# Kernel optimization log

Hardware: AMD Instinct MI355X
Metric: run time of the kernel (lower is better)

## Reference

```python
import jax, jax.numpy as jnp
import numpy as np

D_P, D_T, D_F = 128, 256, 384
D = D_P + D_T + D_F            # 768
NUM_PART, NUM_TIMES, NUM_F0 = 64, 601, 360
NHEAD, NLAYERS, DFF = 12, 6, 2048
CTX, PRED = 1024, 64
BATCH = 8
NEG = -1e9


def sin_emb(vals, d, L, base=10000.0):
    # vectorized version of the per-scalar sin_embedding loop
    i = jnp.arange(d // 2, dtype=jnp.float32)
    wk = base ** (-i / d) * (d / L)
    ang = vals[..., None].astype(jnp.float32) * wk           # [..., d/2]
    return jnp.stack([jnp.sin(ang), jnp.cos(ang)], axis=-1).reshape(vals.shape + (d,))


def layernorm(x, g, b, eps=1e-5):
    mu = jnp.mean(x, axis=-1, keepdims=True)
    var = jnp.var(x, axis=-1, keepdims=True)
    return (x - mu) * jax.lax.rsqrt(var + eps) * g + b


def setup_inputs() -> dict:
    key = jax.random.key(0)
    ks = jax.random.split(key, 20)
    inp = {}
    inp['context_participant'] = jax.random.randint(ks[0], (BATCH, CTX), 0, NUM_PART)
    inp['context_time'] = jax.random.uniform(ks[1], (BATCH, CTX), jnp.float32) * 60.0
    inp['context_f0'] = jax.random.randint(ks[2], (BATCH, CTX), 0, NUM_F0)
    # learned / frozen tables
    inp['part_table'] = jax.random.normal(ks[3], (NUM_PART, D_P), jnp.float32)
    inp['time_table'] = sin_emb(jnp.arange(NUM_TIMES, dtype=jnp.float32), D_T, NUM_TIMES)
    inp['f0_table'] = sin_emb(jnp.arange(NUM_F0, dtype=jnp.float32), D_F, NUM_F0)
    inp['pad'] = jax.random.normal(ks[4], (D,), jnp.float32)
    s = 0.02
    inp['Wqkv'] = jax.random.normal(ks[5], (NLAYERS, 3 * D, D), jnp.float32) * s
    inp['bqkv'] = jnp.zeros((NLAYERS, 3 * D), jnp.float32)
    inp['Wo'] = jax.random.normal(ks[6], (NLAYERS, D, D), jnp.float32) * s
    inp['bo'] = jnp.zeros((NLAYERS, D), jnp.float32)
    inp['ln1_g'] = jnp.ones((NLAYERS, D), jnp.float32)
    inp['ln1_b'] = jnp.zeros((NLAYERS, D), jnp.float32)
    inp['W1'] = jax.random.normal(ks[7], (NLAYERS, DFF, D), jnp.float32) * s
    inp['b1'] = jnp.zeros((NLAYERS, DFF), jnp.float32)
    inp['W2'] = jax.random.normal(ks[8], (NLAYERS, D, DFF), jnp.float32) * s
    inp['b2'] = jnp.zeros((NLAYERS, D), jnp.float32)
    inp['ln2_g'] = jnp.ones((NLAYERS, D), jnp.float32)
    inp['ln2_b'] = jnp.zeros((NLAYERS, D), jnp.float32)
    return inp


def reference(context_participant, context_time, context_f0, part_table, time_table,
              f0_table, pad, Wqkv, bqkv, Wo, bo, ln1_g, ln1_b, W1, b1, W2, b2,
              ln2_g, ln2_b):
    B = context_participant.shape[0]
    emb = jnp.concatenate([
        part_table[context_participant],
        sin_emb(context_time, D_T, NUM_TIMES),
        f0_table[context_f0],
    ], axis=-1)                                               # [B, CTX, D]
    dummy = jnp.broadcast_to(pad[None, None, :], (B, PRED, D))
    x = jnp.concatenate([emb, dummy], axis=1)                 # [B, S, D]
    S = CTX + PRED
    # causal mask with -1e9 above diagonal; target block fully masked (incl. diag)
    mask = jnp.where(jnp.triu(jnp.ones((S, S), bool), k=1), NEG, 0.0).astype(jnp.float32)
    mask = mask.at[CTX:, CTX:].set(NEG)
    hd = D // NHEAD
    scale = 1.0 / jnp.sqrt(jnp.float32(hd))
    for l in range(NLAYERS):
        qkv = x @ Wqkv[l].T + bqkv[l]
        q, k, v = jnp.split(qkv, 3, axis=-1)
        q = q.reshape(B, S, NHEAD, hd)
        k = k.reshape(B, S, NHEAD, hd)
        v = v.reshape(B, S, NHEAD, hd)
        scores = jnp.einsum('bqhd,bkhd->bhqk', q, k) * scale + mask
        attn = jax.nn.softmax(scores, axis=-1)
        ctx = jnp.einsum('bhqk,bkhd->bqhd', attn, v).reshape(B, S, D)
        x = layernorm(x + (ctx @ Wo[l].T + bo[l]), ln1_g[l], ln1_b[l])
        ff = jax.nn.relu(x @ W1[l].T + b1[l]) @ W2[l].T + b2[l]
        x = layernorm(x + ff, ln2_g[l], ln2_b[l])
    pred = x[:, CTX:, :]
    pred_cat_logits = pred[:, :, :D_P] @ part_table.T
    pred_time_logits = pred[:, :, D_P:D_P + D_T] @ time_table.T
    pred_f0_logits = pred[:, :, D_P + D_T:] @ f0_table.T
    return (pred_cat_logits, pred_time_logits, pred_f0_logits)
```

## Files before the change

kernel.cpp:

```cpp
#include <hip/hip_runtime.h>
#include <hip/hip_bf16.h>
#include <math.h>

#define D_P 128
#define D_T 256
#define D_F 384
#define DIM 768
#define NUM_TIMES 601
#define NUM_F0 360
#define NHEAD 12
#define HD 64
#define NLAYERS 6
#define DFF 2048
#define CTX 1024
#define SEQ 1088
#define BATCH 8
#define ROWS (BATCH*SEQ)
#define TDIM3 (3*DIM)
#define PREDROWS 512

typedef unsigned short ushort_t;
typedef __attribute__((ext_vector_type(8))) short bfrag;
typedef __attribute__((ext_vector_type(4))) float f32x4;

__global__ void SequenceModel_30425548325019_kernel(unsigned short* out, int n, unsigned short v) {
  int i = blockIdx.x * 256 + threadIdx.x;
  if (i < n) out[i] = v;
}

__device__ inline short f2bf(float f) {
  unsigned u = __float_as_uint(f);
  unsigned r = (u + 0x7FFFu + ((u >> 16) & 1u)) >> 16;
  return (short)r;
}

__device__ inline void gload16(const void* g, void* l) {
  __builtin_amdgcn_global_load_lds(
      (const __attribute__((address_space(1))) unsigned*)g,
      (__attribute__((address_space(3))) unsigned*)l, 16, 0, 0);
}

__global__ __launch_bounds__(256) void cvt_bf16(const float* __restrict__ src,
                                                ushort_t* __restrict__ dst, int n) {
  int i = (blockIdx.x * 256 + threadIdx.x) * 4;
  if (i >= n) return;
  float4 v = *(const float4*)(src + i);
  dst[i + 0] = (ushort_t)f2bf(v.x);
  dst[i + 1] = (ushort_t)f2bf(v.y);
  dst[i + 2] = (ushort_t)f2bf(v.z);
  dst[i + 3] = (ushort_t)f2bf(v.w);
}

__global__ __launch_bounds__(256) void embed_kernel(
    const int* __restrict__ cp, const float* __restrict__ ct,
    const int* __restrict__ cf, const float* __restrict__ part,
    const float* __restrict__ f0t, const float* __restrict__ pad,
    float* __restrict__ x, ushort_t* __restrict__ xb) {
  int idx = blockIdx.x * 256 + threadIdx.x;
  if (idx >= ROWS * DIM) return;
  int d = idx % DIM;
  int row = idx / DIM;
  int b = row / SEQ, s = row - b * SEQ;
  float v;
  if (s >= CTX) {
    v = pad[d];
  } else if (d < D_P) {
    v = part[cp[b * CTX + s] * D_P + d];
  } else if (d < D_P + D_T) {
    int j = d - D_P;
    int i2 = j >> 1;
    float wk = powf(10000.f, -(float)i2 / (float)D_T) * ((float)D_T / (float)NUM_TIMES);
    float ang = ct[b * CTX + s] * wk;
    v = (j & 1) ? cosf(ang) : sinf(ang);
  } else {
    v = f0t[cf[b * CTX + s] * D_F + (d - D_P - D_T)];
  }
  x[idx] = v;
  xb[idx] = (ushort_t)f2bf(v);
}

#define BM 128
#define BN 128
#define BK 32

__global__ __launch_bounds__(256) void gemm_bb(
    const ushort_t* __restrict__ A, const ushort_t* __restrict__ B,
    const float* __restrict__ bias, const float* __restrict__ resid,
    float* __restrict__ C, ushort_t* __restrict__ Cb,
    int M, int N, int K, int relu, int qscale) {
  __shared__ short As[4 * BM * 8];
  __shared__ short Bs[4 * BN * 8];
  const int tid = threadIdx.x;
  const int wave = tid >> 6, lane = tid & 63;
  const int wr = wave >> 1, wc = wave & 1;
  const int l15 = lane & 15, l4 = lane >> 4;
  const int m0 = blockIdx.y * BM, n0 = blockIdx.x * BN;
  f32x4 acc[4][4] = {};

  for (int k0 = 0; k0 < K; k0 += BK) {
    __syncthreads();
    #pragma unroll
    for (int i = 0; i < 2; ++i) {
      int u = i * 256 + wave * 64 + lane;
      int row = u & 127, kg = u >> 7;
      gload16(A + (size_t)(m0 + row) * K + k0 + kg * 8, &As[(i * 256 + wave * 64) * 8]);
      gload16(B + (size_t)(n0 + row) * K + k0 + kg * 8, &Bs[(i * 256 + wave * 64) * 8]);
    }
    __syncthreads();
    bfrag a[4], b[4];
    #pragma unroll
    for (int f = 0; f < 4; ++f) {
      a[f] = *(const bfrag*)&As[(l4 * BM + wr * 64 + f * 16 + l15) * 8];
      b[f] = *(const bfrag*)&Bs[(l4 * BN + wc * 64 + f * 16 + l15) * 8];
    }
    #pragma unroll
    for (int i = 0; i < 4; ++i)
      #pragma unroll
      for (int j = 0; j < 4; ++j)
        acc[i][j] = __builtin_amdgcn_mfma_f32_16x16x32_bf16(a[i], b[j], acc[i][j], 0, 0, 0);
  }
  #pragma unroll
  for (int i = 0; i < 4; ++i) {
    int mbase = m0 + wr * 64 + i * 16 + l4 * 4;
    #pragma unroll
    for (int j = 0; j < 4; ++j) {
      int n = n0 + wc * 64 + j * 16 + l15;
      float bv = bias[n];
      #pragma unroll
      for (int r = 0; r < 4; ++r) {
        int m = mbase + r;
        float v = acc[i][j][r] + bv;
        if (resid) v += resid[(size_t)m * N + n];
        if (relu) v = fmaxf(v, 0.f);
        if (qscale && n < DIM) v *= 0.125f;
        if (C) C[(size_t)m * N + n] = v;
        if (Cb) Cb[(size_t)m * N + n] = (ushort_t)f2bf(v);
      }
    }
  }
}

__global__ __launch_bounds__(256) void gather_pred(const ushort_t* __restrict__ xb,
                                                   ushort_t* __restrict__ xpb) {
  int idx = blockIdx.x * 256 + threadIdx.x;
  if (idx >= PREDROWS * DIM) return;
  int r = idx / DIM, d = idx - r * DIM;
  int b = r >> 6, rr = r & 63;
  xpb[idx] = xb[(size_t)(b * SEQ + CTX + rr) * DIM + d];
}

__global__ __launch_bounds__(256) void head_mfma(
    const ushort_t* __restrict__ A, const ushort_t* __restrict__ B,
    float* __restrict__ C, int N, int K, int lda, int coloff) {
  __shared__ short As[4 * BM * 8];
  __shared__ short Bs[4 * BN * 8];
  const int tid = threadIdx.x;
  const int wave = tid >> 6, lane = tid & 63;
  const int wr = wave >> 1, wc = wave & 1;
  const int l15 = lane & 15, l4 = lane >> 4;
  const int m0 = blockIdx.y * BM, n0 = blockIdx.x * BN;
  f32x4 acc[4][4] = {};

  for (int k0 = 0; k0 < K; k0 += BK) {
    __syncthreads();
    #pragma unroll
    for (int i = 0; i < 2; ++i) {
      int u = i * 256 + wave * 64 + lane;
      int row = u & 127, kg = u >> 7;
      gload16(A + (size_t)(m0 + row) * lda + coloff + k0 + kg * 8,
              &As[(i * 256 + wave * 64) * 8]);
      gload16(B + (size_t)(n0 + row) * K + k0 + kg * 8,
              &Bs[(i * 256 + wave * 64) * 8]);
    }
    __syncthreads();
    bfrag a[4], b[4];
    #pragma unroll
    for (int f = 0; f < 4; ++f) {
      a[f] = *(const bfrag*)&As[(l4 * BM + wr * 64 + f * 16 + l15) * 8];
      b[f] = *(const bfrag*)&Bs[(l4 * BN + wc * 64 + f * 16 + l15) * 8];
    }
    #pragma unroll
    for (int i = 0; i < 4; ++i)
      #pragma unroll
      for (int j = 0; j < 4; ++j)
        acc[i][j] = __builtin_amdgcn_mfma_f32_16x16x32_bf16(a[i], b[j], acc[i][j], 0, 0, 0);
  }
  #pragma unroll
  for (int i = 0; i < 4; ++i) {
    int mbase = m0 + wr * 64 + i * 16 + l4 * 4;
    #pragma unroll
    for (int j = 0; j < 4; ++j) {
      int n = n0 + wc * 64 + j * 16 + l15;
      if (n >= N) continue;
      #pragma unroll
      for (int r = 0; r < 4; ++r)
        C[(size_t)(mbase + r) * N + n] = acc[i][j][r];
    }
  }
}

#define QBLK 64
#define KBLK 64
__global__ __launch_bounds__(256) void attn_mfma(const ushort_t* __restrict__ qkv,
                                                 ushort_t* __restrict__ outb) {
  const int qt = blockIdx.x, h = blockIdx.y, b = blockIdx.z;
  const int q0 = qt * QBLK;
  __shared__ short Vt[8 * 64 * 9];
  __shared__ short Ps[8 * 64 * 9];
  __shared__ float SO[64 * 65];
  __shared__ float alphaS[64], linvS[64];
  const int tid = threadIdx.x;
  const int wave = tid >> 6, lane = tid & 63;
  const int l15 = lane & 15, l4 = lane >> 4;
  const int smrow = tid >> 2, smc = tid & 3;
  const int qf = wave;

  const size_t qrow_addr = (size_t)(b * SEQ + q0 + qf * 16 + l15) * TDIM3 + h * HD;
  bfrag aq0 = *(const bfrag*)(qkv + qrow_addr + 0 * 32 + l4 * 8);
  bfrag aq1 = *(const bfrag*)(qkv + qrow_addr + 1 * 32 + l4 * 8);

  float mrun = -1e30f, lrun = 0.f;
  f32x4 o[4] = {};
  const int nkt = (q0 < CTX) ? (q0 + QBLK) / KBLK : (CTX / KBLK);

  for (int kt = 0; kt < nkt; ++kt) {
    const int k0 = kt * KBLK;
    __syncthreads();
    #pragma unroll
    for (int i = 0; i < 2; ++i) {
      int u = tid + 256 * i;
      int krow = u >> 3, dg = u & 7;
      bfrag vv = *(const bfrag*)(qkv + (size_t)(b * SEQ + k0 + krow) * TDIM3 + 2 * DIM + h * HD + dg * 8);
      int kg = krow >> 3, j = krow & 7;
      #pragma unroll
      for (int e = 0; e < 8; ++e)
        Vt[(kg * 64 + dg * 8 + e) * 9 + j] = vv[e];
    }
    #pragma unroll
    for (int jk = 0; jk < 4; ++jk) {
      const size_t krow_addr = (size_t)(b * SEQ + k0 + jk * 16 + l15) * TDIM3 + DIM + h * HD;
      bfrag bk0 = *(const bfrag*)(qkv + krow_addr + 0 * 32 + l4 * 8);
      bfrag bk1 = *(const bfrag*)(qkv + krow_addr + 1 * 32 + l4 * 8);
      f32x4 s = {};
      s = __builtin_amdgcn_mfma_f32_16x16x32_bf16(aq0, bk0, s, 0, 0, 0);
      s = __builtin_amdgcn_mfma_f32_16x16x32_bf16(aq1, bk1, s, 0, 0, 0);
      #pragma unroll
      for (int r = 0; r < 4; ++r)
        SO[(qf * 16 + l4 * 4 + r) * 65 + jk * 16 + l15] = s[r];
    }
    __syncthreads();
    {
      const int qglob = q0 + smrow;
      float p[16];
      float tm = -1e30f;
      #pragma unroll
      for (int i = 0; i < 16; ++i) {
        int kg = k0 + smc * 16 + i;
        float s = SO[smrow * 65 + smc * 16 + i];
        bool allowed = (qglob < CTX) ? (kg <= qglob) : true;
        p[i] = allowed ? s : -1e30f;
        tm = fmaxf(tm, p[i]);
      }
      tm = fmaxf(tm, __shfl_xor(tm, 1));
      tm = fmaxf(tm, __shfl_xor(tm, 2));
      float mn = fmaxf(mrun, tm);
      float alpha = __expf(mrun - mn);
      float ls = 0.f;
      #pragma unroll
      for (int i = 0; i < 16; ++i) { p[i] = __expf(p[i] - mn); ls += p[i]; }
      ls += __shfl_xor(ls, 1);
      ls += __shfl_xor(ls, 2);
      lrun = lrun * alpha + ls;
      mrun = mn;
      if (smc == 0) alphaS[smrow] = alpha;
      short* pd0 = &Ps[((smc * 2 + 0) * 64 + smrow) * 9];
      short* pd1 = &Ps[((smc * 2 + 1) * 64 + smrow) * 9];
      #pragma unroll
      for (int i = 0; i < 8; ++i) { pd0[i] = f2bf(p[i]); pd1[i] = f2bf(p[i + 8]); }
    }
    __syncthreads();
    {
      #pragma unroll
      for (int r = 0; r < 4; ++r) {
        float ar = alphaS[qf * 16 + l4 * 4 + r];
        #pragma unroll
        for (int df = 0; df < 4; ++df) o[df][r] *= ar;
      }
      #pragma unroll
      for (int c = 0; c < 2; ++c) {
        bfrag pa = *(const bfrag*)&Ps[((c * 4 + l4) * 64 + qf * 16 + l15) * 9];
        #pragma unroll
        for (int df = 0; df < 4; ++df) {
          bfrag v = *(const bfrag*)&Vt[((c * 4 + l4) * 64 + df * 16 + l15) * 9];
          o[df] = __builtin_amdgcn_mfma_f32_16x16x32_bf16(pa, v, o[df], 0, 0, 0);
        }
      }
    }
  }
  if (smc == 0) linvS[smrow] = 1.f / lrun;
  __syncthreads();
  #pragma unroll
  for (int r = 0; r < 4; ++r) {
    float li = linvS[qf * 16 + l4 * 4 + r];
    #pragma unroll
    for (int df = 0; df < 4; ++df)
      SO[(qf * 16 + l4 * 4 + r) * 65 + df * 16 + l15] = o[df][r] * li;
  }
  __syncthreads();
  #pragma unroll
  for (int i = 0; i < 2; ++i) {
    int s = tid + 256 * i;
    int r = s >> 3, kg = s & 7;
    ushort_t* dst = outb + (size_t)(b * SEQ + q0 + r) * DIM + h * HD + kg * 8;
    const float* sp = &SO[r * 65 + kg * 8];
    bfrag t;
    #pragma unroll
    for (int e = 0; e < 8; ++e) t[e] = f2bf(sp[e]);
    *(bfrag*)dst = t;
  }
}

__global__ __launch_bounds__(256) void ln_kernel(float* __restrict__ x,
                                                 const float* __restrict__ g,
                                                 const float* __restrict__ bb,
                                                 ushort_t* __restrict__ xb) {
  const int row = blockIdx.x;
  float* p = x + (size_t)row * DIM;
  ushort_t* pb = xb + (size_t)row * DIM;
  const int tid = threadIdx.x;
  float v0 = p[tid], v1 = p[tid + 256], v2 = p[tid + 512];
  float s1 = v0 + v1 + v2;
  float s2 = v0 * v0 + v1 * v1 + v2 * v2;
  #pragma unroll
  for (int off = 32; off >= 1; off >>= 1) {
    s1 += __shfl_down(s1, off);
    s2 += __shfl_down(s2, off);
  }
  __shared__ float r1[4], r2[4];
  int wid = tid >> 6;
  if ((tid & 63) == 0) { r1[wid] = s1; r2[wid] = s2; }
  __syncthreads();
  s1 = r1[0] + r1[1] + r1[2] + r1[3];
  s2 = r2[0] + r2[1] + r2[2] + r2[3];
  const float mu = s1 * (1.f / DIM);
  const float var = s2 * (1.f / DIM) - mu * mu;
  const float rs = rsqrtf(var + 1e-5f);
  float o0 = (v0 - mu) * rs * g[tid]       + bb[tid];
  float o1 = (v1 - mu) * rs * g[tid + 256] + bb[tid + 256];
  float o2 = (v2 - mu) * rs * g[tid + 512] + bb[tid + 512];
  p[tid] = o0;       pb[tid] = (ushort_t)f2bf(o0);
  p[tid + 256] = o1; pb[tid + 256] = (ushort_t)f2bf(o1);
  p[tid + 512] = o2; pb[tid + 512] = (ushort_t)f2bf(o2);
}

extern "C" void kernel_launch(void* const* d_in, const int* in_sizes, int n_in,
                              void* d_out, int out_size, void* d_ws, size_t ws_size,
                              hipStream_t stream) {
  const size_t N_X    = (size_t)ROWS * DIM;
  const size_t N_XB   = N_X / 2;
  const size_t N_BUFB = (size_t)ROWS * TDIM3 / 2;
  const size_t N_CTB  = N_X / 2;
  const size_t N_WQ   = 10616832 / 2;
  const size_t N_WO   = 3538944 / 2;
  const size_t N_W1   = 9437184 / 2;
  const size_t N_W2   = 9437184 / 2;
  const size_t N_PT   = 8192 / 2;
  const size_t N_TT   = 153856 / 2;
  const size_t N_FT   = 138240 / 2;
  const size_t N_XPB  = (size_t)PREDROWS * DIM / 2;
  size_t need = (N_X + N_XB + N_BUFB + N_CTB + N_WQ + N_WO + N_W1 + N_W2 +
                 N_PT + N_TT + N_FT + N_XPB) * sizeof(float);
  if (ws_size < need) {
    SequenceModel_30425548325019_kernel<<<(out_size + 255) / 256, 256, 0, stream>>>(
        (unsigned short*)d_out, out_size, (unsigned short)0x4280);
    return;
  }

  const int*   cp    = (const int*)d_in[0];
  const float* ct    = (const float*)d_in[1];
  const int*   cf    = (const int*)d_in[2];
  const float* part  = (const float*)d_in[3];
  const float* timet = (const float*)d_in[4];
  const float* f0t   = (const float*)d_in[5];
  const float* pad   = (const float*)d_in[6];
  const float* Wqkv  = (const float*)d_in[7];
  const float* bqkv  = (const float*)d_in[8];
  const float* Wo    = (const float*)d_in[9];
  const float* bo    = (const float*)d_in[10];
  const float* ln1g  = (const float*)d_in[11];
  const float* ln1b  = (const float*)d_in[12];
  const float* W1    = (const float*)d_in[13];
  const float* b1    = (const float*)d_in[14];
  const float* W2    = (const float*)d_in[15];
  const float* b2    = (const float*)d_in[16];
  const float* ln2g  = (const float*)d_in[17];
  const float* ln2b  = (const float*)d_in[18];

  float* base = (float*)d_ws;
  float*    x      = base;                 base += N_X;
  ushort_t* xb     = (ushort_t*)base;      base += N_XB;
  ushort_t* bufb   = (ushort_t*)base;      base += N_BUFB;
  ushort_t* ctxbb  = (ushort_t*)base;      base += N_CTB;
  ushort_t* Wqkvb  = (ushort_t*)base;      base += N_WQ;
  ushort_t* Wob    = (ushort_t*)base;      base += N_WO;
  ushort_t* W1b    = (ushort_t*)base;      base += N_W1;
  ushort_t* W2b    = (ushort_t*)base;      base += N_W2;
  ushort_t* partb  = (ushort_t*)base;      base += N_PT;
  ushort_t* timetb = (ushort_t*)base;      base += N_TT;
  ushort_t* f0tb   = (ushort_t*)base;      base += N_FT;
  ushort_t* xpb    = (ushort_t*)base;

  cvt_bf16<<<(10616832 / 4 + 255) / 256, 256, 0, stream>>>(Wqkv, Wqkvb, 10616832);
  cvt_bf16<<<(3538944 / 4 + 255) / 256, 256, 0, stream>>>(Wo, Wob, 3538944);
  cvt_bf16<<<(9437184 / 4 + 255) / 256, 256, 0, stream>>>(W1, W1b, 9437184);
  cvt_bf16<<<(9437184 / 4 + 255) / 256, 256, 0, stream>>>(W2, W2b, 9437184);
  cvt_bf16<<<(8192 / 4 + 255) / 256, 256, 0, stream>>>(part, partb, 8192);
  cvt_bf16<<<(153856 / 4 + 255) / 256, 256, 0, stream>>>(timet, timetb, 153856);
  cvt_bf16<<<(138240 / 4 + 255) / 256, 256, 0, stream>>>(f0t, f0tb, 138240);

  embed_kernel<<<(ROWS * DIM + 255) / 256, 256, 0, stream>>>(cp, ct, cf, part, f0t, pad, x, xb);

  for (int l = 0; l < NLAYERS; ++l) {
    gemm_bb<<<dim3(TDIM3 / BN, ROWS / BM), 256, 0, stream>>>(
        xb, Wqkvb + (size_t)l * TDIM3 * DIM, bqkv + l * TDIM3, nullptr,
        nullptr, bufb, ROWS, TDIM3, DIM, 0, 1);
    attn_mfma<<<dim3(SEQ / QBLK, NHEAD, BATCH), 256, 0, stream>>>(bufb, ctxbb);
    gemm_bb<<<dim3(DIM / BN, ROWS / BM), 256, 0, stream>>>(
        ctxbb, Wob + (size_t)l * DIM * DIM, bo + l * DIM, x,
        x, nullptr, ROWS, DIM, DIM, 0, 0);
    ln_kernel<<<ROWS, 256, 0, stream>>>(x, ln1g + l * DIM, ln1b + l * DIM, xb);
    gemm_bb<<<dim3(DFF / BN, ROWS / BM), 256, 0, stream>>>(
        xb, W1b + (size_t)l * DFF * DIM, b1 + l * DFF, nullptr,
        nullptr, bufb, ROWS, DFF, DIM, 1, 0);
    gemm_bb<<<dim3(DIM / BN, ROWS / BM), 256, 0, stream>>>(
        bufb, W2b + (size_t)l * DIM * DFF, b2 + l * DIM, x,
        x, nullptr, ROWS, DIM, DFF, 0, 0);
    ln_kernel<<<ROWS, 256, 0, stream>>>(x, ln2g + l * DIM, ln2b + l * DIM, xb);
  }

  float* out = (float*)d_out;
  gather_pred<<<(PREDROWS * DIM + 255) / 256, 256, 0, stream>>>(xb, xpb);
  head_mfma<<<dim3(1, PREDROWS / BM), 256, 0, stream>>>(xpb, partb, out, 64, 128, DIM, 0);
  head_mfma<<<dim3(5, PREDROWS / BM), 256, 0, stream>>>(xpb, timetb, out + 32768, NUM_TIMES, 256, DIM, 128);
  head_mfma<<<dim3(3, PREDROWS / BM), 256, 0, stream>>>(xpb, f0tb, out + 32768 + 307712, NUM_F0, 384, DIM, 384);
}
```

Baseline: 3.069 ms.

## Double-buffer K tiles in LDS and prefetch V; remap attention blocks per XCD

The attention kernel now prefetches the next K tile into a double-buffered LDS array with async global-to-LDS loads and preloads the next V tile into registers while the current tile is computed, aiming to hide global load latency. The grid is flattened to 1D and block indices are remapped so blocks of the same (batch, head) land on the same XCD, which should improve L2 reuse of K/V. It adds 16KB of LDS and extra registers, which may lower occupancy.

```diff
diff --git a/kernel.cpp b/kernel.cpp
--- a/kernel.cpp
+++ b/kernel.cpp
@@ -203,8 +203,15 @@
 #define KBLK 64
 __global__ __launch_bounds__(256) void attn_mfma(const ushort_t* __restrict__ qkv,
                                                  ushort_t* __restrict__ outb) {
-  const int qt = blockIdx.x, h = blockIdx.y, b = blockIdx.z;
+  const int bid = blockIdx.x;
+  const int xcd = bid & 7;
+  const int r0 = bid >> 3;
+  const int qt = r0 % 17;
+  const int g = (r0 / 17) * 8 + xcd;
+  const int h = g % NHEAD, b = g / NHEAD;
   const int q0 = qt * QBLK;
+
+  __shared__ short Ks2[2][8 * 64 * 8];
   __shared__ short Vt[8 * 64 * 9];
   __shared__ short Ps[8 * 64 * 9];
   __shared__ float SO[64 * 65];
@@ -216,37 +223,68 @@
   const int qf = wave;
 
   const size_t qrow_addr = (size_t)(b * SEQ + q0 + qf * 16 + l15) * TDIM3 + h * HD;
-  bfrag aq0 = *(const bfrag*)(qkv + qrow_addr + 0 * 32 + l4 * 8);
-  bfrag aq1 = *(const bfrag*)(qkv + qrow_addr + 1 * 32 + l4 * 8);
-
+  bfrag aq0 = *(const bfrag*)(qkv + qrow_addr + l4 * 8);
+  bfrag aq1 = *(const bfrag*)(qkv + qrow_addr + 32 + l4 * 8);
+
+  const int nkt = (q0 < CTX) ? (q0 + QBLK) / KBLK : (CTX / KBLK);
+
+  bfrag vA0, vA1, vB0, vB1;
+  {
+    #pragma unroll
+    for (int i = 0; i < 2; ++i) {
+      int u = tid + 256 * i;
+      int kg = u >> 6, row = u & 63;
+      gload16(qkv + (size_t)(b * SEQ + row) * TDIM3 + DIM + h * HD + kg * 8,
+              &Ks2[0][(i * 256 + wave * 64) * 8]);
+      int krow = u >> 3, dg = u & 7;
+      bfrag vv = *(const bfrag*)(qkv + (size_t)(b * SEQ + krow) * TDIM3 + 2 * DIM + h * HD + dg * 8);
+      if (i == 0) vA0 = vv; else vA1 = vv;
+    }
+  }
   float mrun = -1e30f, lrun = 0.f;
   f32x4 o[4] = {};
-  const int nkt = (q0 < CTX) ? (q0 + QBLK) / KBLK : (CTX / KBLK);
 
   for (int kt = 0; kt < nkt; ++kt) {
     const int k0 = kt * KBLK;
+    const int cur = kt & 1;
     __syncthreads();
     #pragma unroll
     for (int i = 0; i < 2; ++i) {
       int u = tid + 256 * i;
       int krow = u >> 3, dg = u & 7;
-      bfrag vv = *(const bfrag*)(qkv + (size_t)(b * SEQ + k0 + krow) * TDIM3 + 2 * DIM + h * HD + dg * 8);
-      int kg = krow >> 3, j = krow & 7;
+      int kg2 = krow >> 3, j = krow & 7;
+      bfrag vv = cur ? (i == 0 ? vB0 : vB1) : (i == 0 ? vA0 : vA1);
       #pragma unroll
       for (int e = 0; e < 8; ++e)
-        Vt[(kg * 64 + dg * 8 + e) * 9 + j] = vv[e];
-    }
-    #pragma unroll
-    for (int jk = 0; jk < 4; ++jk) {
-      const size_t krow_addr = (size_t)(b * SEQ + k0 + jk * 16 + l15) * TDIM3 + DIM + h * HD;
-      bfrag bk0 = *(const bfrag*)(qkv + krow_addr + 0 * 32 + l4 * 8);
-      bfrag bk1 = *(const bfrag*)(qkv + krow_addr + 1 * 32 + l4 * 8);
-      f32x4 s = {};
-      s = __builtin_amdgcn_mfma_f32_16x16x32_bf16(aq0, bk0, s, 0, 0, 0);
-      s = __builtin_amdgcn_mfma_f32_16x16x32_bf16(aq1, bk1, s, 0, 0, 0);
-      #pragma unroll
-      for (int r = 0; r < 4; ++r)
-        SO[(qf * 16 + l4 * 4 + r) * 65 + jk * 16 + l15] = s[r];
+        Vt[(kg2 * 64 + dg * 8 + e) * 9 + j] = vv[e];
+    }
+    if (kt + 1 < nkt) {
+      const int k1 = k0 + KBLK;
+      #pragma unroll
+      for (int i = 0; i < 2; ++i) {
+        int u = tid + 256 * i;
+        int kg = u >> 6, row = u & 63;
+        gload16(qkv + (size_t)(b * SEQ + k1 + row) * TDIM3 + DIM + h * HD + kg * 8,
+                &Ks2[1 - cur][(i * 256 + wave * 64) * 8]);
+        int krow = u >> 3, dg = u & 7;
+        bfrag nv = *(const bfrag*)(qkv + (size_t)(b * SEQ + k1 + krow) * TDIM3 + 2 * DIM + h * HD + dg * 8);
+        if (cur) { if (i == 0) vA0 = nv; else vA1 = nv; }
+        else     { if (i == 0) vB0 = nv; else vB1 = nv; }
+      }
+    }
+    {
+      const short* Kc = &Ks2[cur][0];
+      #pragma unroll
+      for (int jk = 0; jk < 4; ++jk) {
+        bfrag bk0 = *(const bfrag*)&Kc[((0 * 4 + l4) * 64 + jk * 16 + l15) * 8];
+        bfrag bk1 = *(const bfrag*)&Kc[((1 * 4 + l4) * 64 + jk * 16 + l15) * 8];
+        f32x4 s = {};
+        s = __builtin_amdgcn_mfma_f32_16x16x32_bf16(aq0, bk0, s, 0, 0, 0);
+        s = __builtin_amdgcn_mfma_f32_16x16x32_bf16(aq1, bk1, s, 0, 0, 0);
+        #pragma unroll
+        for (int r = 0; r < 4; ++r)
+          SO[(qf * 16 + l4 * 4 + r) * 65 + jk * 16 + l15] = s[r];
+      }
     }
     __syncthreads();
     {
@@ -424,7 +462,7 @@
     gemm_bb<<<dim3(TDIM3 / BN, ROWS / BM), 256, 0, stream>>>(
         xb, Wqkvb + (size_t)l * TDIM3 * DIM, bqkv + l * TDIM3, nullptr,
         nullptr, bufb, ROWS, TDIM3, DIM, 0, 1);
-    attn_mfma<<<dim3(SEQ / QBLK, NHEAD, BATCH), 256, 0, stream>>>(bufb, ctxbb);
+    attn_mfma<<<dim3(17 * NHEAD * BATCH), 256, 0, stream>>>(bufb, ctxbb);
     gemm_bb<<<dim3(DIM / BN, ROWS / BM), 256, 0, stream>>>(
         ctxbb, Wob + (size_t)l * DIM * DIM, bo + l * DIM, x,
         x, nullptr, ROWS, DIM, DIM, 0, 0);
```

Result: slower. 3.136 ms (+2.2%).

## Double-buffer GEMM shared tiles and remap attention blocks for XCD locality

Applied to the files above, without the earlier changes.

The GEMM kernel now keeps two LDS buffers and issues the global-to-LDS loads for the next K tile before running MFMAs on the current one, leaving one barrier per iteration instead of two. The attention launch becomes a 1D grid whose block index is decoded so that all query tiles of one (batch, head) pair go to the same XCD, which should improve L2 reuse of K/V. The cost is double the LDS footprint in the GEMM, which may lower occupancy.

```diff
diff --git a/kernel.cpp b/kernel.cpp
--- a/kernel.cpp
+++ b/kernel.cpp
@@ -88,8 +88,8 @@
     const float* __restrict__ bias, const float* __restrict__ resid,
     float* __restrict__ C, ushort_t* __restrict__ Cb,
     int M, int N, int K, int relu, int qscale) {
-  __shared__ short As[4 * BM * 8];
-  __shared__ short Bs[4 * BN * 8];
+  __shared__ short As[2][4 * BM * 8];
+  __shared__ short Bs[2][4 * BN * 8];
   const int tid = threadIdx.x;
   const int wave = tid >> 6, lane = tid & 63;
   const int wr = wave >> 1, wc = wave & 1;
@@ -97,27 +97,42 @@
   const int m0 = blockIdx.y * BM, n0 = blockIdx.x * BN;
   f32x4 acc[4][4] = {};
 
+  const int u0row = (wave * 64 + lane) & 127, u0kg = (wave * 64 + lane) >> 7;
+  const int u1row = (256 + wave * 64 + lane) & 127, u1kg = (256 + wave * 64 + lane) >> 7;
+  const ushort_t* Ap0 = A + (size_t)(m0 + u0row) * K + u0kg * 8;
+  const ushort_t* Bp0 = B + (size_t)(n0 + u0row) * K + u0kg * 8;
+  const ushort_t* Ap1 = A + (size_t)(m0 + u1row) * K + u1kg * 8;
+  const ushort_t* Bp1 = B + (size_t)(n0 + u1row) * K + u1kg * 8;
+  const int ldsoff0 = (wave * 64) * 8;
+  const int ldsoff1 = (256 + wave * 64) * 8;
+
+  gload16(Ap0, &As[0][ldsoff0]);
+  gload16(Bp0, &Bs[0][ldsoff0]);
+  gload16(Ap1, &As[0][ldsoff1]);
+  gload16(Bp1, &Bs[0][ldsoff1]);
+  __syncthreads();
+
+  int cur = 0;
   for (int k0 = 0; k0 < K; k0 += BK) {
-    __syncthreads();
-    #pragma unroll
-    for (int i = 0; i < 2; ++i) {
-      int u = i * 256 + wave * 64 + lane;
-      int row = u & 127, kg = u >> 7;
-      gload16(A + (size_t)(m0 + row) * K + k0 + kg * 8, &As[(i * 256 + wave * 64) * 8]);
-      gload16(B + (size_t)(n0 + row) * K + k0 + kg * 8, &Bs[(i * 256 + wave * 64) * 8]);
-    }
-    __syncthreads();
+    if (k0 + BK < K) {
+      gload16(Ap0 + k0 + BK, &As[cur ^ 1][ldsoff0]);
+      gload16(Bp0 + k0 + BK, &Bs[cur ^ 1][ldsoff0]);
+      gload16(Ap1 + k0 + BK, &As[cur ^ 1][ldsoff1]);
+      gload16(Bp1 + k0 + BK, &Bs[cur ^ 1][ldsoff1]);
+    }
     bfrag a[4], b[4];
     #pragma unroll
     for (int f = 0; f < 4; ++f) {
-      a[f] = *(const bfrag*)&As[(l4 * BM + wr * 64 + f * 16 + l15) * 8];
-      b[f] = *(const bfrag*)&Bs[(l4 * BN + wc * 64 + f * 16 + l15) * 8];
+      a[f] = *(const bfrag*)&As[cur][(l4 * BM + wr * 64 + f * 16 + l15) * 8];
+      b[f] = *(const bfrag*)&Bs[cur][(l4 * BN + wc * 64 + f * 16 + l15) * 8];
     }
     #pragma unroll
     for (int i = 0; i < 4; ++i)
       #pragma unroll
       for (int j = 0; j < 4; ++j)
         acc[i][j] = __builtin_amdgcn_mfma_f32_16x16x32_bf16(a[i], b[j], acc[i][j], 0, 0, 0);
+    __syncthreads();
+    cur ^= 1;
   }
   #pragma unroll
   for (int i = 0; i < 4; ++i) {
@@ -203,8 +218,14 @@
 #define KBLK 64
 __global__ __launch_bounds__(256) void attn_mfma(const ushort_t* __restrict__ qkv,
                                                  ushort_t* __restrict__ outb) {
-  const int qt = blockIdx.x, h = blockIdx.y, b = blockIdx.z;
+  const int bid = blockIdx.x;
+  const int xcd = bid & 7;
+  const int r0 = bid >> 3;
+  const int qt = r0 % 17;
+  const int g = (r0 / 17) * 8 + xcd;
+  const int h = g % NHEAD, b = g / NHEAD;
   const int q0 = qt * QBLK;
+
   __shared__ short Vt[8 * 64 * 9];
   __shared__ short Ps[8 * 64 * 9];
   __shared__ float SO[64 * 65];
@@ -216,8 +237,8 @@
   const int qf = wave;
 
   const size_t qrow_addr = (size_t)(b * SEQ + q0 + qf * 16 + l15) * TDIM3 + h * HD;
-  bfrag aq0 = *(const bfrag*)(qkv + qrow_addr + 0 * 32 + l4 * 8);
-  bfrag aq1 = *(const bfrag*)(qkv + qrow_addr + 1 * 32 + l4 * 8);
+  bfrag aq0 = *(const bfrag*)(qkv + qrow_addr + l4 * 8);
+  bfrag aq1 = *(const bfrag*)(qkv + qrow_addr + 32 + l4 * 8);
 
   float mrun = -1e30f, lrun = 0.f;
   f32x4 o[4] = {};
@@ -239,8 +260,8 @@
     #pragma unroll
     for (int jk = 0; jk < 4; ++jk) {
       const size_t krow_addr = (size_t)(b * SEQ + k0 + jk * 16 + l15) * TDIM3 + DIM + h * HD;
-      bfrag bk0 = *(const bfrag*)(qkv + krow_addr + 0 * 32 + l4 * 8);
-      bfrag bk1 = *(const bfrag*)(qkv + krow_addr + 1 * 32 + l4 * 8);
+      bfrag bk0 = *(const bfrag*)(qkv + krow_addr + l4 * 8);
+      bfrag bk1 = *(const bfrag*)(qkv + krow_addr + 32 + l4 * 8);
       f32x4 s = {};
       s = __builtin_amdgcn_mfma_f32_16x16x32_bf16(aq0, bk0, s, 0, 0, 0);
       s = __builtin_amdgcn_mfma_f32_16x16x32_bf16(aq1, bk1, s, 0, 0, 0);
@@ -424,7 +445,7 @@
     gemm_bb<<<dim3(TDIM3 / BN, ROWS / BM), 256, 0, stream>>>(
         xb, Wqkvb + (size_t)l * TDIM3 * DIM, bqkv + l * TDIM3, nullptr,
         nullptr, bufb, ROWS, TDIM3, DIM, 0, 1);
-    attn_mfma<<<dim3(SEQ / QBLK, NHEAD, BATCH), 256, 0, stream>>>(bufb, ctxbb);
+    attn_mfma<<<dim3(17 * NHEAD * BATCH), 256, 0, stream>>>(bufb, ctxbb);
     gemm_bb<<<dim3(DIM / BN, ROWS / BM), 256, 0, stream>>>(
         ctxbb, Wob + (size_t)l * DIM * DIM, bo + l * DIM, x,
         x, nullptr, ROWS, DIM, DIM, 0, 0);
```

After: 3.145 ms. +2.5%, slower.
